# Optimization experiments

Measured on AMD Instinct MI355X. Metric: run time of the kernel, lower is better.

Reference implementation:

```python
import jax, jax.numpy as jnp
import numpy as np

B, L, D, H = 2, 2048, 1024, 16
HD = D // H


def setup_inputs() -> dict:
    key = jax.random.key(0)
    ks = jax.random.split(key, 8)
    x = jax.random.normal(ks[0], (B, L, D), dtype=jnp.float32)
    WQ = jax.random.normal(ks[1], (D, D), dtype=jnp.float32) * 0.02
    bQ = jnp.zeros((D,), dtype=jnp.float32)
    WK = jax.random.normal(ks[2], (D, D), dtype=jnp.float32) * 0.02
    bK = jnp.zeros((D,), dtype=jnp.float32)
    WV = jax.random.normal(ks[3], (D, D), dtype=jnp.float32) * 0.02
    bV = jnp.zeros((D,), dtype=jnp.float32)
    Wc = jax.random.normal(ks[4], (D, D), dtype=jnp.float32) * 0.02  # dense channel-mix matrix [d_out, d_in]
    return {"x": x, "WQ": WQ, "bQ": bQ, "WK": WK, "bK": bK, "WV": WV, "bV": bV, "Wc": Wc}


def reference(x, WQ, bQ, WK, bK, WV, bV, Wc):
    b, l, d = x.shape
    # --- TokenMixWeightGenerator (LOW_RANK): T = softmax(causal(Q K^T / sqrt(hd)))
    q = (x @ WQ.T + bQ).reshape(b, l, H, HD).transpose(0, 2, 1, 3)  # [B,H,L,hd]
    k = (x @ WK.T + bK).reshape(b, l, H, HD).transpose(0, 2, 1, 3)  # [B,H,L,hd]
    scores = jnp.einsum("bhid,bhjd->bhij", q, k) / jnp.sqrt(jnp.float32(HD))
    causal_mask = jnp.tril(jnp.ones((l, l), dtype=bool))  # keep j <= i
    scores = jnp.where(causal_mask, scores, -jnp.inf)
    T = jax.nn.softmax(scores, axis=-1)  # [B,H,L,L] explicit token-mix matrix
    # --- UnifiedFeaturizer (expansion=1): V reshaped per head
    v = (x @ WV.T + bV).reshape(b, l, H, HD).transpose(0, 2, 1, 3)  # [B,H,L,hd]
    # --- Y = C @ (T @ V)
    mixed = jnp.einsum("bhij,bhjd->bhid", T, v)  # [B,H,L,hd]
    mixed = mixed.transpose(0, 2, 1, 3).reshape(b, l, d)  # [B,L,D]
    y = mixed @ Wc.T  # channel mixing: output = input @ W.T
    return y
```

## Files before the change

kernel.cpp:

```cpp
#include <hip/hip_runtime.h>


typedef __bf16 bf16x8 __attribute__((ext_vector_type(8)));
typedef float f32x4 __attribute__((ext_vector_type(4)));
typedef float f32x16 __attribute__((ext_vector_type(16)));
typedef unsigned short us4 __attribute__((ext_vector_type(4)));

#if defined(__has_builtin)
#if __has_builtin(__builtin_amdgcn_global_load_lds)
#define HAS_GLL 1
#endif
#if __has_builtin(__builtin_amdgcn_exp2f)
#define EXP2F(x) __builtin_amdgcn_exp2f(x)
#endif
#endif
#ifndef HAS_GLL
#define HAS_GLL 0
#endif
#ifndef EXP2F
#define EXP2F(x) exp2f(x)
#endif

__device__ __forceinline__ float bf2f(unsigned short u) {
    union { unsigned int i; float f; } v; v.i = ((unsigned int)u) << 16; return v.f;
}
__device__ __forceinline__ unsigned short f2bf(float f) {
    union { float f; unsigned int i; } v; v.f = f;
    unsigned int r = v.i + 0x7FFFu + ((v.i >> 16) & 1u);
    return (unsigned short)(r >> 16);
}
__device__ __forceinline__ f32x4 mfma16(bf16x8 a, bf16x8 b, f32x4 c) {
    return __builtin_amdgcn_mfma_f32_16x16x32_bf16(a, b, c, 0, 0, 0);
}
__device__ __forceinline__ f32x16 mfma32(bf16x8 a, bf16x8 b, f32x16 c) {
    return __builtin_amdgcn_mfma_f32_32x32x16_bf16(a, b, c, 0, 0, 0);
}
__device__ __forceinline__ float clamp4(float v) {
    return fminf(fmaxf(v, -1e4f), 1e4f);
}
union U8 { unsigned short s[8]; bf16x8 v; };

__device__ __forceinline__ unsigned int cvt_pk_bf16(float lo, float hi) {
    unsigned int r;
    asm("v_cvt_pk_bf16_f32 %0, %1, %2" : "=v"(r) : "v"(lo), "v"(hi));
    return r;
}
__device__ __forceinline__ void pl32swap(unsigned int& a, unsigned int& b) {
    asm volatile("v_permlane32_swap_b32 %0, %1" : "+v"(a), "+v"(b));
}

#if HAS_GLL
__device__ __forceinline__ void gl_lds16(const unsigned short* g, unsigned short* l) {
    __builtin_amdgcn_global_load_lds(
        (const __attribute__((address_space(1))) void*)g,
        (__attribute__((address_space(3))) void*)l, 16, 0, 0);
}
#endif


__global__ __launch_bounds__(256) void convert_all(
    const float* __restrict__ x, const float* __restrict__ WQ,
    const float* __restrict__ WK, const float* __restrict__ WV,
    const float* __restrict__ Wc,
    unsigned short* __restrict__ xbf, unsigned short* __restrict__ wbf)
{
    size_t e = ((size_t)blockIdx.x * 256 + threadIdx.x) * 8;
    const float* src; unsigned short* dst; size_t off;
    if (e < 4194304) { src = x; dst = xbf; off = e; }
    else {
        size_t j = e - 4194304; int sel = (int)(j >> 20); off = j & 1048575;
        src = (sel == 0) ? WQ : (sel == 1) ? WK : (sel == 2) ? WV : Wc;
        dst = wbf + (size_t)sel * 1048576;
    }
    f32x4 a = *(const f32x4*)(src + off);
    f32x4 b = *(const f32x4*)(src + off + 4);
    U8 u;
    u.s[0] = f2bf(a[0]); u.s[1] = f2bf(a[1]); u.s[2] = f2bf(a[2]); u.s[3] = f2bf(a[3]);
    u.s[4] = f2bf(b[0]); u.s[5] = f2bf(b[1]); u.s[6] = f2bf(b[2]); u.s[7] = f2bf(b[3]);
    *(bf16x8*)(dst + off) = u.v;
}

__global__ __launch_bounds__(256) void gemm128(
    const unsigned short* __restrict__ A, const unsigned short* __restrict__ Wbase,
    const float* __restrict__ b0, const float* __restrict__ b1, const float* __restrict__ b2,
    void* __restrict__ d0, void* __restrict__ d1, void* __restrict__ d2, int modeBase)
{
    const int z = blockIdx.z;
    const unsigned short* W = Wbase + (size_t)z * 1048576;
    const float* bias = (z == 0) ? b0 : (z == 1) ? b1 : b2;
    void* dst = (z == 0) ? d0 : (z == 1) ? d1 : d2;
    const int mode = modeBase + z;

    __shared__ __align__(16) unsigned short At[128][32];
    __shared__ __align__(16) unsigned short Bt[128][32];

    const int mb = blockIdx.y * 128, nb = blockIdx.x * 128;
    const int tid = threadIdx.x, w = tid >> 6, lane = tid & 63;
    const int wr = w >> 1, wc = w & 1;
    const int col = lane & 15, quad = lane >> 4;

    f32x4 acc[4][4];
    for (int i = 0; i < 4; ++i) for (int j = 0; j < 4; ++j) acc[i][j] = (f32x4){0.f, 0.f, 0.f, 0.f};

#if HAS_GLL
    const unsigned short* ga = A + (size_t)(mb + w * 32 + (lane >> 2)) * 1024 + (lane & 3) * 8;
    const unsigned short* gw = W + (size_t)(nb + w * 32 + (lane >> 2)) * 1024 + (lane & 3) * 8;
    unsigned short* lA0 = &At[w * 32][0];
    unsigned short* lA1 = &At[w * 32 + 16][0];
    unsigned short* lB0 = &Bt[w * 32][0];
    unsigned short* lB1 = &Bt[w * 32 + 16][0];
#else
    const int srow = w * 32 + (lane >> 1);
    const int scol = (lane & 1) * 16;
    const unsigned short* Ab = A + (size_t)(mb + srow) * 1024 + scol;
    const unsigned short* Wb = W + (size_t)(nb + srow) * 1024 + scol;
#endif

    for (int kb = 0; kb < 1024; kb += 32) {
#if HAS_GLL
        gl_lds16(ga + kb, lA0);
        gl_lds16(ga + kb + 16 * 1024, lA1);
        gl_lds16(gw + kb, lB0);
        gl_lds16(gw + kb + 16 * 1024, lB1);
#else
        *(bf16x8*)&At[srow][scol]     = *(const bf16x8*)(Ab + kb);
        *(bf16x8*)&At[srow][scol + 8] = *(const bf16x8*)(Ab + kb + 8);
        *(bf16x8*)&Bt[srow][scol]     = *(const bf16x8*)(Wb + kb);
        *(bf16x8*)&Bt[srow][scol + 8] = *(const bf16x8*)(Wb + kb + 8);
#endif
        __syncthreads();
        bf16x8 a[4], b[4];
        for (int i = 0; i < 4; ++i) a[i] = *(const bf16x8*)&At[wr * 64 + i * 16 + col][quad * 8];
        for (int j = 0; j < 4; ++j) b[j] = *(const bf16x8*)&Bt[wc * 64 + j * 16 + col][quad * 8];
        for (int i = 0; i < 4; ++i)
            for (int j = 0; j < 4; ++j)
                acc[i][j] = mfma16(a[i], b[j], acc[i][j]);
        __syncthreads();
    }

    for (int i = 0; i < 4; ++i) {
        const int mbase = mb + wr * 64 + i * 16 + quad * 4;
        const int bb = mbase >> 11, l = mbase & 2047;
        for (int j = 0; j < 4; ++j) {
            const int n = nb + wc * 64 + j * 16 + col;
            const float bv = bias ? bias[n] : 0.f;
            if (mode == 3) {
                float* o = (float*)dst;
                for (int r = 0; r < 4; ++r)
                    o[(size_t)(mbase + r) * 1024 + n] = clamp4(acc[i][j][r] + bv);
            } else if (mode == 2) {
                const int h = n >> 6, hd = n & 63;
                us4 pk;
                for (int r = 0; r < 4; ++r) pk[r] = f2bf(clamp4(acc[i][j][r] + bv));
                *(us4*)((unsigned short*)dst + (size_t)(bb * 16 + h) * 131072
                        + (size_t)hd * 2048 + l) = pk;
            } else {
                const int h = n >> 6, hd = n & 63;
                unsigned short* o = (unsigned short*)dst + (size_t)(bb * 16 + h) * 131072
                                    + (size_t)l * 64 + hd;
                for (int r = 0; r < 4; ++r)
                    o[(size_t)r * 64] = f2bf(clamp4(acc[i][j][r] + bv));
            }
        }
    }
}


template<bool DIAG>
__device__ __forceinline__ void soft_pack(
    const f32x16& sacc, bf16x8* pa, float& lpart, int kg0, int qg)
{
    float p[16];
#pragma unroll
    for (int r = 0; r < 16; ++r) {
        float v = sacc[r] * 0.18033688f;
        if (DIAG) {
            int kg = kg0 + (r & 3) + 8 * (r >> 2);
            if (kg > qg) v = -1e30f;
        }
        v = fminf(v, 86.5f);
        p[r] = EXP2F(v);
    }
    float t0 = (p[0] + p[1]) + (p[2] + p[3]);
    float t1 = (p[4] + p[5]) + (p[6] + p[7]);
    float t2 = (p[8] + p[9]) + (p[10] + p[11]);
    float t3 = (p[12] + p[13]) + (p[14] + p[15]);
    lpart += (t0 + t1) + (t2 + t3);
#pragma unroll
    for (int c = 0; c < 2; ++c) {
        unsigned int a0 = cvt_pk_bf16(p[8*c + 0], p[8*c + 1]);
        unsigned int b0 = cvt_pk_bf16(p[8*c + 4], p[8*c + 5]);
        unsigned int a1 = cvt_pk_bf16(p[8*c + 2], p[8*c + 3]);
        unsigned int b1 = cvt_pk_bf16(p[8*c + 6], p[8*c + 7]);
        pl32swap(a0, b0);
        pl32swap(a1, b1);
        union PW { unsigned int w[4]; bf16x8 v; } pw;
        pw.w[0] = a0; pw.w[1] = a1; pw.w[2] = b0; pw.w[3] = b1;
        pa[c] = pw.v;
    }
}

template<bool DIAG>
__device__ __forceinline__ void attn32_step2(
    const unsigned short (*__restrict__ Kt)[72], const unsigned short* __restrict__ Vt,
    const bf16x8* __restrict__ qf, f32x16* __restrict__ oacc, float& lpart,
    int kb, int qg, int hi, int c31)
{
    f32x16 s0, s1;
#pragma unroll
    for (int r = 0; r < 16; ++r) { s0[r] = 0.f; s1[r] = 0.f; }
#pragma unroll
    for (int dc = 0; dc < 4; ++dc) {
        bf16x8 kf0 = *(const bf16x8*)&Kt[c31][dc * 16 + hi * 8];
        bf16x8 kf1 = *(const bf16x8*)&Kt[32 + c31][dc * 16 + hi * 8];
        s0 = mfma32(kf0, qf[dc], s0);
        s1 = mfma32(kf1, qf[dc], s1);
    }
    bf16x8 pa[4];
    soft_pack<DIAG>(s0, pa,     lpart, kb + 4 * hi,      qg);
    soft_pack<DIAG>(s1, pa + 2, lpart, kb + 32 + 4 * hi, qg);
#pragma unroll
    for (int b2 = 0; b2 < 2; ++b2)
#pragma unroll
        for (int kc = 0; kc < 4; ++kc) {
            bf16x8 vf = *(const bf16x8*)&Vt[(size_t)(b2 * 32 + c31) * 136 + kc * 16 + hi * 8];
            oacc[b2] = mfma32(pa[kc], vf, oacc[b2]);
        }
}

__device__ __forceinline__ void attn_write32(
    unsigned short* __restrict__ mixed, int gb, int h, int q0, int c31, int hi,
    const f32x16* __restrict__ oacc, const float* __restrict__ lrow)
{
    f32x4 iv[4];
#pragma unroll
    for (int m = 0; m < 4; ++m) {
        f32x4 lv = *(const f32x4*)&lrow[4 * hi + 8 * m];
#pragma unroll
        for (int r = 0; r < 4; ++r) iv[m][r] = 1.f / lv[r];
    }
#pragma unroll
    for (int b2 = 0; b2 < 2; ++b2)
#pragma unroll
        for (int r = 0; r < 16; ++r) {
            const int qrow = q0 + 4 * hi + (r & 3) + 8 * (r >> 2);
            const float val = clamp4(oacc[b2][r] * iv[r >> 2][r & 3]);
            mixed[(size_t)(gb * 2048 + qrow) * 1024 + h * 64 + b2 * 32 + c31] = f2bf(val);
        }
}

__global__ __launch_bounds__(256, 2) void attn32d(
    const unsigned short* __restrict__ Q, const unsigned short* __restrict__ K,
    const unsigned short* __restrict__ V, unsigned short* __restrict__ mixed)
{
    const int lb = blockIdx.x;
    const int i = lb & 255, kk = lb >> 8;
    const int bh = i & 31, j = i >> 5;
    const int A = kk ? (15 - j) : j;
    const int niter = A + 1;

    const int tid = threadIdx.x, w = tid >> 6, lane = tid & 63;
    const int c31 = lane & 31, hi = lane >> 5;

    __shared__ __align__(16) unsigned short Kt[128][72];
    __shared__ __align__(16) unsigned short Vt[64][136];
    __shared__ __align__(16) float lslab[4][32];

    const unsigned short* Qb = Q + (size_t)bh * 131072;
    const unsigned short* Kb = K + (size_t)bh * 131072;
    const unsigned short* Vb = V + (size_t)bh * 131072;

    const int q0 = A * 128 + w * 32;
    const int qg = q0 + c31;
    const int ss = 2 * A + (w >> 1);

    bf16x8 qf[4];
    {
        const unsigned short* Qr = Qb + (size_t)qg * 64 + hi * 8;
#pragma unroll
        for (int dc = 0; dc < 4; ++dc) qf[dc] = *(const bf16x8*)(Qr + dc * 16);
    }

    f32x16 oacc[2];
#pragma unroll
    for (int b2 = 0; b2 < 2; ++b2)
#pragma unroll
        for (int r = 0; r < 16; ++r) oacc[b2][r] = 0.f;
    float lpart = 0.f;

    const int sr = tid >> 3, sc = (tid & 7) * 8;

    const unsigned short* kp = Kb + (size_t)sr * 64 + sc;
    const unsigned short* vp = Vb + (size_t)sr * 2048 + sc;
    bf16x8 pk0 = *(const bf16x8*)kp;
    bf16x8 pk1 = *(const bf16x8*)(kp + 32 * 64);
    bf16x8 pk2 = *(const bf16x8*)(kp + 64 * 64);
    bf16x8 pk3 = *(const bf16x8*)(kp + 96 * 64);
    bf16x8 pv0 = *(const bf16x8*)vp;
    bf16x8 pv1 = *(const bf16x8*)(vp + 32 * 2048);
    bf16x8 pv2 = *(const bf16x8*)(vp + 64);
    bf16x8 pv3 = *(const bf16x8*)(vp + 32 * 2048 + 64);

    for (int jj = 0; jj < niter; ++jj) {
        __syncthreads();
        *(bf16x8*)&Kt[sr][sc]       = pk0;
        *(bf16x8*)&Kt[sr + 32][sc]  = pk1;
        *(bf16x8*)&Kt[sr + 64][sc]  = pk2;
        *(bf16x8*)&Kt[sr + 96][sc]  = pk3;
        *(bf16x8*)&Vt[sr][sc]       = pv0;
        *(bf16x8*)&Vt[sr + 32][sc]  = pv1;
        *(bf16x8*)&Vt[sr][64 + sc]  = pv2;
        *(bf16x8*)&Vt[sr + 32][64 + sc] = pv3;
        __syncthreads();
        if (jj + 1 < niter) {
            const int kb2 = (jj + 1) * 128;
            const unsigned short* kp2 = Kb + (size_t)(kb2 + sr) * 64 + sc;
            const unsigned short* vp2 = Vb + (size_t)sr * 2048 + kb2 + sc;
            pk0 = *(const bf16x8*)kp2;
            pk1 = *(const bf16x8*)(kp2 + 32 * 64);
            pk2 = *(const bf16x8*)(kp2 + 64 * 64);
            pk3 = *(const bf16x8*)(kp2 + 96 * 64);
            pv0 = *(const bf16x8*)vp2;
            pv1 = *(const bf16x8*)(vp2 + 32 * 2048);
            pv2 = *(const bf16x8*)(vp2 + 64);
            pv3 = *(const bf16x8*)(vp2 + 32 * 2048 + 64);
        }
        const int t0 = 2 * jj, t1 = t0 + 1;
        if (t0 < ss)
            attn32_step2<false>(&Kt[0], &Vt[0][0],  qf, oacc, lpart, t0 * 64, qg, hi, c31);
        else if (t0 == ss)
            attn32_step2<true >(&Kt[0], &Vt[0][0],  qf, oacc, lpart, t0 * 64, qg, hi, c31);
        if (t1 < ss)
            attn32_step2<false>(&Kt[64], &Vt[0][64], qf, oacc, lpart, t1 * 64, qg, hi, c31);
        else if (t1 == ss)
            attn32_step2<true >(&Kt[64], &Vt[0][64], qf, oacc, lpart, t1 * 64, qg, hi, c31);
    }

    float ltot = lpart + __shfl_xor(lpart, 32, 64);
    if (lane < 32) lslab[w][lane] = ltot;

    const int gb = bh >> 4, h = bh & 15;
    attn_write32(mixed, gb, h, q0, c31, hi, oacc, &lslab[w][0]);
}


__device__ __forceinline__ bf16x8 load8(const void* base, size_t eoff, int asF32) {
    if (asF32) {
        const float* p = (const float*)base + eoff;
        f32x4 a = *(const f32x4*)p;
        f32x4 b = *(const f32x4*)(p + 4);
        U8 u;
        u.s[0]=f2bf(a[0]); u.s[1]=f2bf(a[1]); u.s[2]=f2bf(a[2]); u.s[3]=f2bf(a[3]);
        u.s[4]=f2bf(b[0]); u.s[5]=f2bf(b[1]); u.s[6]=f2bf(b[2]); u.s[7]=f2bf(b[3]);
        return u.v;
    }
    return *(const bf16x8*)((const unsigned short*)base + eoff);
}

__global__ void dtype_probe(const unsigned short* __restrict__ x, int* __restrict__ flag) {
    if (threadIdx.x == 0) {
        int c = 0;
        for (int i = 0; i < 128; ++i) {
            int e = (x[2 * i] >> 7) & 0xFF;
            if (e >= 100 && e <= 135) ++c;
        }
        *flag = (c < 64) ? 1 : 0;
    }
}

__global__ __launch_bounds__(256) void gemm_bt(
    const void* __restrict__ Ap, const void* __restrict__ Wp,
    const void* __restrict__ biasp, void* __restrict__ dout,
    unsigned short* __restrict__ wsdst, const int* __restrict__ flag,
    long aOff, long outOff, int mode, int aFlagged)
{
    const int f32 = *flag;
    __shared__ __align__(16) unsigned short At[64][32];
    __shared__ __align__(16) unsigned short Bt[64][32];
    const int mb = blockIdx.y * 64, nb = blockIdx.x * 64;
    const int tid = threadIdx.x;
    const int w = tid >> 6, lane = tid & 63;
    const int wr = w >> 1, wc = w & 1;
    const int col = lane & 15, quad = lane >> 4;
    const int srow = tid >> 2, schunk = (tid & 3) * 8;
    const int aF = aFlagged && f32;

    f32x4 acc[2][2];
    for (int i = 0; i < 2; ++i) for (int j = 0; j < 2; ++j) acc[i][j] = (f32x4){0.f,0.f,0.f,0.f};

    const size_t aBase = (size_t)aOff + (size_t)(mb + srow) * 1024 + schunk;
    const size_t wBase = (size_t)(nb + srow) * 1024 + schunk;

    for (int kb = 0; kb < 1024; kb += 32) {
        *(bf16x8*)(&At[srow][schunk]) = load8(Ap, aBase + kb, aF);
        *(bf16x8*)(&Bt[srow][schunk]) = load8(Wp, wBase + kb, f32);
        __syncthreads();
        bf16x8 a0 = *(const bf16x8*)(&At[wr * 32 + col][quad * 8]);
        bf16x8 a1 = *(const bf16x8*)(&At[wr * 32 + 16 + col][quad * 8]);
        bf16x8 b0 = *(const bf16x8*)(&Bt[wc * 32 + col][quad * 8]);
        bf16x8 b1 = *(const bf16x8*)(&Bt[wc * 32 + 16 + col][quad * 8]);
        acc[0][0] = mfma16(a0, b0, acc[0][0]);
        acc[0][1] = mfma16(a0, b1, acc[0][1]);
        acc[1][0] = mfma16(a1, b0, acc[1][0]);
        acc[1][1] = mfma16(a1, b1, acc[1][1]);
        __syncthreads();
    }

    for (int mi = 0; mi < 2; ++mi) {
        for (int ni = 0; ni < 2; ++ni) {
            int n = nb + wc * 32 + ni * 16 + col;
            float bv = 0.f;
            if (biasp) bv = f32 ? ((const float*)biasp)[n] : bf2f(((const unsigned short*)biasp)[n]);
            for (int r = 0; r < 4; ++r) {
                int m = mb + wr * 32 + mi * 16 + quad * 4 + r;
                float v = clamp4(acc[mi][ni][r] + bv);
                if (mode == 3) {
                    size_t idx = (size_t)outOff + (size_t)m * 1024 + n;
                    if (f32) ((float*)dout)[idx] = v;
                    else     ((unsigned short*)dout)[idx] = f2bf(v);
                } else {
                    int h = n >> 6, hd = n & 63;
                    size_t idx = (mode == 2)
                        ? (size_t)h * 131072 + (size_t)hd * 2048 + m
                        : (size_t)h * 131072 + (size_t)m * 64 + hd;
                    unsigned short* dstp = (mode == 0)
                        ? (unsigned short*)dout + (f32 ? 4194304 : 2097152)
                        : wsdst;
                    dstp[idx] = f2bf(v);
                }
            }
        }
    }
}

__global__ __launch_bounds__(256) void attn_kernel(
    const void* __restrict__ dout, const unsigned short* __restrict__ Kw,
    const unsigned short* __restrict__ Vw, unsigned short* __restrict__ mixed,
    const int* __restrict__ flag)
{
    const int f32 = *flag;
    const int qtile = blockIdx.x;
    const int h = blockIdx.y;
    const int w = threadIdx.x >> 6, lane = threadIdx.x & 63;
    const int col = lane & 15, quad = lane >> 4;

    __shared__ __align__(16) unsigned short Plds[4][16][64];

    const unsigned short* Qs = (const unsigned short*)dout + (f32 ? 4194304 : 2097152);
    const unsigned short* Qb = Qs + (size_t)h * 131072;
    const unsigned short* Kb = Kw + (size_t)h * 131072;
    const unsigned short* Vb = Vw + (size_t)h * 131072;

    const int q0 = qtile * 64 + w * 16;
    bf16x8 aq0 = *(const bf16x8*)(Qb + (size_t)(q0 + col) * 64 + quad * 8);
    bf16x8 aq1 = *(const bf16x8*)(Qb + (size_t)(q0 + col) * 64 + 32 + quad * 8);

    float m_run[4] = {-1e30f, -1e30f, -1e30f, -1e30f};
    float l_run[4] = {0.f, 0.f, 0.f, 0.f};
    f32x4 oacc[4];
    for (int i = 0; i < 4; ++i) oacc[i] = (f32x4){0.f, 0.f, 0.f, 0.f};

    for (int kt = 0; kt <= qtile; ++kt) {
        const int kb = kt * 64;
        f32x4 s[4];
        for (int t = 0; t < 4; ++t) {
            s[t] = (f32x4){0.f, 0.f, 0.f, 0.f};
            bf16x8 bk0 = *(const bf16x8*)(Kb + (size_t)(kb + t * 16 + col) * 64 + quad * 8);
            bf16x8 bk1 = *(const bf16x8*)(Kb + (size_t)(kb + t * 16 + col) * 64 + 32 + quad * 8);
            s[t] = mfma16(aq0, bk0, s[t]);
            s[t] = mfma16(aq1, bk1, s[t]);
        }
        for (int t = 0; t < 4; ++t)
            for (int r = 0; r < 4; ++r) {
                float v = clamp4(s[t][r] * 0.125f);
                if (kt == qtile && (t * 16 + col > w * 16 + quad * 4 + r)) v = -1e30f;
                s[t][r] = v;
            }
        float mt[4];
        for (int r = 0; r < 4; ++r)
            mt[r] = fmaxf(fmaxf(s[0][r], s[1][r]), fmaxf(s[2][r], s[3][r]));
        for (int off = 1; off < 16; off <<= 1)
            for (int r = 0; r < 4; ++r)
                mt[r] = fmaxf(mt[r], __shfl_xor(mt[r], off, 64));
        float alpha[4], rs[4], p[4][4];
        for (int r = 0; r < 4; ++r) {
            float mn = fmaxf(m_run[r], mt[r]);
            alpha[r] = __expf(m_run[r] - mn);
            m_run[r] = mn;
        }
        for (int t = 0; t < 4; ++t)
            for (int r = 0; r < 4; ++r)
                p[t][r] = __expf(s[t][r] - m_run[r]);
        for (int r = 0; r < 4; ++r)
            rs[r] = (p[0][r] + p[1][r]) + (p[2][r] + p[3][r]);
        for (int off = 1; off < 16; off <<= 1)
            for (int r = 0; r < 4; ++r)
                rs[r] += __shfl_xor(rs[r], off, 64);
        for (int r = 0; r < 4; ++r)
            l_run[r] = l_run[r] * alpha[r] + rs[r];
        for (int nt = 0; nt < 4; ++nt)
            for (int r = 0; r < 4; ++r)
                oacc[nt][r] *= alpha[r];
        for (int t = 0; t < 4; ++t)
            for (int r = 0; r < 4; ++r)
                Plds[w][quad * 4 + r][t * 16 + col] = f2bf(p[t][r]);
        __syncthreads();
        bf16x8 ap0 = *(const bf16x8*)(&Plds[w][col][quad * 8]);
        bf16x8 ap1 = *(const bf16x8*)(&Plds[w][col][32 + quad * 8]);
        for (int nt = 0; nt < 4; ++nt) {
            bf16x8 bv0 = *(const bf16x8*)(Vb + (size_t)(nt * 16 + col) * 2048 + kb + quad * 8);
            bf16x8 bv1 = *(const bf16x8*)(Vb + (size_t)(nt * 16 + col) * 2048 + kb + 32 + quad * 8);
            oacc[nt] = mfma16(ap0, bv0, oacc[nt]);
            oacc[nt] = mfma16(ap1, bv1, oacc[nt]);
        }
        __syncthreads();
    }

    float inv[4];
    for (int r = 0; r < 4; ++r) inv[r] = 1.f / l_run[r];
    for (int nt = 0; nt < 4; ++nt)
        for (int r = 0; r < 4; ++r) {
            int qrow = q0 + quad * 4 + r;
            mixed[(size_t)qrow * 1024 + h * 64 + nt * 16 + col] = f2bf(clamp4(oacc[nt][r] * inv[r]));
        }
}


extern "C" void kernel_launch(void* const* d_in, const int* in_sizes, int n_in,
                              void* d_out, int out_size, void* d_ws, size_t ws_size,
                              hipStream_t stream) {
    (void)in_sizes; (void)n_in; (void)out_size;
    const void* x  = d_in[0];
    const void* WQ = d_in[1]; const void* bQ = d_in[2];
    const void* WK = d_in[3]; const void* bK = d_in[4];
    const void* WV = d_in[5]; const void* bV = d_in[6];
    const void* Wc = d_in[7];

    if (ws_size >= (size_t)32 * 1024 * 1024) {
        unsigned short* wbf   = (unsigned short*)d_ws;
        unsigned short* Kst   = wbf + 4194304;
        unsigned short* VTst  = Kst + 4194304;
        unsigned short* mixed = VTst + 4194304;
        unsigned short* xbf   = (unsigned short*)d_out;
        unsigned short* Qst   = xbf + 4194304;

        convert_all<<<4096, 256, 0, stream>>>(
            (const float*)x, (const float*)WQ, (const float*)WK,
            (const float*)WV, (const float*)Wc, xbf, wbf);

        gemm128<<<dim3(8, 32, 3), 256, 0, stream>>>(
            xbf, wbf, (const float*)bQ, (const float*)bK, (const float*)bV,
            Qst, Kst, VTst, 0);

        attn32d<<<dim3(512, 1), 256, 0, stream>>>(Qst, Kst, VTst, mixed);

        gemm128<<<dim3(8, 32, 1), 256, 0, stream>>>(
            mixed, wbf + 3145728, nullptr, nullptr, nullptr,
            d_out, nullptr, nullptr, 3);
    } else {
        unsigned short* wsK = (unsigned short*)d_ws;
        unsigned short* wsV = wsK + 2097152;
        unsigned short* wsM = wsV + 2097152;
        int* flag = (int*)((char*)d_ws + 12 * 1024 * 1024);

        dtype_probe<<<1, 64, 0, stream>>>((const unsigned short*)x, flag);

        dim3 gg(16, 32), gb(256);
        for (int b = 0; b < 2; ++b) {
            long xo = (long)b * 2048 * 1024;
            gemm_bt<<<gg, gb, 0, stream>>>(x, WQ, bQ, d_out, nullptr, flag, xo, 0, 0, 1);
            gemm_bt<<<gg, gb, 0, stream>>>(x, WK, bK, d_out, wsK, flag, xo, 0, 1, 1);
            gemm_bt<<<gg, gb, 0, stream>>>(x, WV, bV, d_out, wsV, flag, xo, 0, 2, 1);
            attn_kernel<<<dim3(32, 16), 256, 0, stream>>>(d_out, wsK, wsV, wsM, flag);
            gemm_bt<<<gg, gb, 0, stream>>>(wsM, Wc, nullptr, d_out, nullptr, flag,
                                           0, (long)b * 2048 * 1024, 3, 0);
        }
    }
}
```

Before: 183.9 us.

## Double-buffer LDS tiles in projection GEMM to overlap loads with MFMA

Splits the shared-memory A/B tiles of the 128x128 GEMM into two buffers and prefetches the next K-slice with global-to-LDS loads while the current slice is multiplied. This removes one of the two barriers per K step and is meant to hide global load latency behind MFMA work. It doubles the LDS footprint (32 KB per block), which may reduce occupancy. The correctness of the single barrier depends on when the async global-to-LDS loads complete relative to the wait that barrier emits.

```diff
diff --git a/kernel.cpp b/kernel.cpp
--- a/kernel.cpp
+++ b/kernel.cpp
@@ -91,8 +91,8 @@
     void* dst = (z == 0) ? d0 : (z == 1) ? d1 : d2;
     const int mode = modeBase + z;
 
-    __shared__ __align__(16) unsigned short At[128][32];
-    __shared__ __align__(16) unsigned short Bt[128][32];
+    __shared__ __align__(16) unsigned short At[2][128][32];
+    __shared__ __align__(16) unsigned short Bt[2][128][32];
 
     const int mb = blockIdx.y * 128, nb = blockIdx.x * 128;
     const int tid = threadIdx.x, w = tid >> 6, lane = tid & 63;
@@ -102,41 +102,80 @@
     f32x4 acc[4][4];
     for (int i = 0; i < 4; ++i) for (int j = 0; j < 4; ++j) acc[i][j] = (f32x4){0.f, 0.f, 0.f, 0.f};
 
+    unsigned short* Ab0 = &At[0][0][0];
+    unsigned short* Bb0 = &Bt[0][0][0];
+
 #if HAS_GLL
     const unsigned short* ga = A + (size_t)(mb + w * 32 + (lane >> 2)) * 1024 + (lane & 3) * 8;
     const unsigned short* gw = W + (size_t)(nb + w * 32 + (lane >> 2)) * 1024 + (lane & 3) * 8;
-    unsigned short* lA0 = &At[w * 32][0];
-    unsigned short* lA1 = &At[w * 32 + 16][0];
-    unsigned short* lB0 = &Bt[w * 32][0];
-    unsigned short* lB1 = &Bt[w * 32 + 16][0];
+    const int wbase = w * 1024;
+
+    gl_lds16(ga, Ab0 + wbase);
+    gl_lds16(ga + 16 * 1024, Ab0 + wbase + 512);
+    gl_lds16(gw, Bb0 + wbase);
+    gl_lds16(gw + 16 * 1024, Bb0 + wbase + 512);
+    __syncthreads();
+
+    for (int t = 0; t < 32; ++t) {
+        const int cur = (t & 1) * 4096, nxt = 4096 - cur;
+        if (t + 1 < 32) {
+            const int kb = (t + 1) * 32;
+            gl_lds16(ga + kb, Ab0 + nxt + wbase);
+            gl_lds16(ga + kb + 16 * 1024, Ab0 + nxt + wbase + 512);
+            gl_lds16(gw + kb, Bb0 + nxt + wbase);
+            gl_lds16(gw + kb + 16 * 1024, Bb0 + nxt + wbase + 512);
+        }
+        const unsigned short* Ac = Ab0 + cur;
+        const unsigned short* Bc = Bb0 + cur;
+        bf16x8 a[4], b[4];
+#pragma unroll
+        for (int i = 0; i < 4; ++i) a[i] = *(const bf16x8*)(Ac + (wr * 64 + i * 16 + col) * 32 + quad * 8);
+#pragma unroll
+        for (int j = 0; j < 4; ++j) b[j] = *(const bf16x8*)(Bc + (wc * 64 + j * 16 + col) * 32 + quad * 8);
+#pragma unroll
+        for (int i = 0; i < 4; ++i)
+#pragma unroll
+            for (int j = 0; j < 4; ++j)
+                acc[i][j] = mfma16(a[i], b[j], acc[i][j]);
+        __syncthreads();
+    }
 #else
     const int srow = w * 32 + (lane >> 1);
     const int scol = (lane & 1) * 16;
-    const unsigned short* Ab = A + (size_t)(mb + srow) * 1024 + scol;
-    const unsigned short* Wb = W + (size_t)(nb + srow) * 1024 + scol;
-#endif
-
-    for (int kb = 0; kb < 1024; kb += 32) {
-#if HAS_GLL
-        gl_lds16(ga + kb, lA0);
-        gl_lds16(ga + kb + 16 * 1024, lA1);
-        gl_lds16(gw + kb, lB0);
-        gl_lds16(gw + kb + 16 * 1024, lB1);
-#else
-        *(bf16x8*)&At[srow][scol]     = *(const bf16x8*)(Ab + kb);
-        *(bf16x8*)&At[srow][scol + 8] = *(const bf16x8*)(Ab + kb + 8);
-        *(bf16x8*)&Bt[srow][scol]     = *(const bf16x8*)(Wb + kb);
-        *(bf16x8*)&Bt[srow][scol + 8] = *(const bf16x8*)(Wb + kb + 8);
-#endif
-        __syncthreads();
+    const unsigned short* Abp = A + (size_t)(mb + srow) * 1024 + scol;
+    const unsigned short* Wbp = W + (size_t)(nb + srow) * 1024 + scol;
+    const int soff = srow * 32 + scol;
+
+    *(bf16x8*)(Ab0 + soff)     = *(const bf16x8*)(Abp);
+    *(bf16x8*)(Ab0 + soff + 8) = *(const bf16x8*)(Abp + 8);
+    *(bf16x8*)(Bb0 + soff)     = *(const bf16x8*)(Wbp);
+    *(bf16x8*)(Bb0 + soff + 8) = *(const bf16x8*)(Wbp + 8);
+    __syncthreads();
+
+    for (int t = 0; t < 32; ++t) {
+        const int cur = (t & 1) * 4096, nxt = 4096 - cur;
+        if (t + 1 < 32) {
+            const int kb = (t + 1) * 32;
+            *(bf16x8*)(Ab0 + nxt + soff)     = *(const bf16x8*)(Abp + kb);
+            *(bf16x8*)(Ab0 + nxt + soff + 8) = *(const bf16x8*)(Abp + kb + 8);
+            *(bf16x8*)(Bb0 + nxt + soff)     = *(const bf16x8*)(Wbp + kb);
+            *(bf16x8*)(Bb0 + nxt + soff + 8) = *(const bf16x8*)(Wbp + kb + 8);
+        }
+        const unsigned short* Ac = Ab0 + cur;
+        const unsigned short* Bc = Bb0 + cur;
         bf16x8 a[4], b[4];
-        for (int i = 0; i < 4; ++i) a[i] = *(const bf16x8*)&At[wr * 64 + i * 16 + col][quad * 8];
-        for (int j = 0; j < 4; ++j) b[j] = *(const bf16x8*)&Bt[wc * 64 + j * 16 + col][quad * 8];
+#pragma unroll
+        for (int i = 0; i < 4; ++i) a[i] = *(const bf16x8*)(Ac + (wr * 64 + i * 16 + col) * 32 + quad * 8);
+#pragma unroll
+        for (int j = 0; j < 4; ++j) b[j] = *(const bf16x8*)(Bc + (wc * 64 + j * 16 + col) * 32 + quad * 8);
+#pragma unroll
         for (int i = 0; i < 4; ++i)
+#pragma unroll
             for (int j = 0; j < 4; ++j)
                 acc[i][j] = mfma16(a[i], b[j], acc[i][j]);
         __syncthreads();
     }
+#endif
 
     for (int i = 0; i < 4; ++i) {
         const int mbase = mb + wr * 64 + i * 16 + quad * 4;
```

Result: slower. 191.3 us (+4.1%).
